# Performance work log

Measured on AMD Instinct MI355X. Metric: run time of the kernel, lower is better.

## Reference

```python
import jax, jax.numpy as jnp
import numpy as np

S = 2048       # seq_len
D = 1024       # d_model
H = 16         # heads
DK = 64        # d_k = d_v = D // H


def setup_inputs() -> dict:
    key = jax.random.key(0)
    ks = jax.random.split(key, 12)
    sc_in = 1.0 / np.sqrt(D)
    return {
        "Q": jax.random.normal(ks[0], (S, D), jnp.float32),
        "K": jax.random.normal(ks[1], (S, D), jnp.float32),
        "V": jax.random.normal(ks[2], (S, D), jnp.float32),
        # stacked per-head projection weights (torch Linear math: x @ W + b, W stored [in,out])
        "Wq": jax.random.normal(ks[3], (H, D, DK), jnp.float32) * sc_in,
        "bq": jnp.zeros((H, DK), jnp.float32),
        "Wk": jax.random.normal(ks[4], (H, D, DK), jnp.float32) * sc_in,
        "bk": jnp.zeros((H, DK), jnp.float32),
        "Wv": jax.random.normal(ks[5], (H, D, DK), jnp.float32) * sc_in,
        "bv": jnp.zeros((H, DK), jnp.float32),
        "Wo": jax.random.normal(ks[6], (H * DK, D), jnp.float32) * (1.0 / np.sqrt(H * DK)),
        "bo": jnp.zeros((D,), jnp.float32),
    }


def reference(Q, K, V, Wq, bq, Wk, bk, Wv, bv, Wo, bo):
    # per-head projections, all heads at once: [S,D] x [H,D,DK] -> [H,S,DK]
    q = jnp.einsum("sd,hdk->hsk", Q, Wq) + bq[:, None, :]
    k = jnp.einsum("sd,hdk->hsk", K, Wk) + bk[:, None, :]
    v = jnp.einsum("sd,hdk->hsk", V, Wv) + bv[:, None, :]
    # scaled dot-product attention per head: [H,S,S]
    scores = jnp.einsum("hsk,htk->hst", q, k) / jnp.sqrt(jnp.asarray(DK, q.dtype))
    attn = jax.nn.softmax(scores, axis=-1)
    heads = jnp.einsum("hst,htv->hsv", attn, v)          # [H,S,DK]
    concat = heads.transpose(1, 0, 2).reshape(S, H * DK)  # [S, H*DK]
    return concat @ Wo + bo                               # [S, D]
```

## Files before the change

kernel.cpp:

```cpp
#include <hip/hip_runtime.h>
#include <stdint.h>

#define S_LEN 2048
#define D_MODEL 1024
#define NH 16
#define DKV 64

typedef unsigned short u16;
typedef __bf16 bf16x8 __attribute__((ext_vector_type(8)));
typedef float f32x4 __attribute__((ext_vector_type(4)));

__device__ __forceinline__ u16 f2bf(float f) {
  union { float f; uint32_t u; } v; v.f = f;
  uint32_t r = v.u + 0x7FFFu + ((v.u >> 16) & 1u);
  return (u16)(r >> 16);
}
__device__ __forceinline__ uint32_t pkbf(float lo, float hi) {
  union { float f; uint32_t u; } a, b; a.f = lo; b.f = hi;
  return ((b.u + 0x8000u) & 0xFFFF0000u) | ((a.u + 0x8000u) >> 16);
}
__device__ __forceinline__ void gl16(const u16* g, u16* l) {
  __builtin_amdgcn_global_load_lds(
      (const __attribute__((address_space(1))) unsigned int*)g,
      (__attribute__((address_space(3))) unsigned int*)l, 16, 0, 0);
}

__global__ __launch_bounds__(256) void prep_k(
    const float* __restrict__ Q, const float* __restrict__ K,
    const float* __restrict__ V, const float* __restrict__ Wq,
    const float* __restrict__ Wk, const float* __restrict__ Wv,
    const float* __restrict__ Wo, u16* __restrict__ QKVb,
    u16* __restrict__ Wqt, u16* __restrict__ Wkt, u16* __restrict__ Wvt,
    u16* __restrict__ Wot) {
  __shared__ float tile[32][33];
  const int idx = blockIdx.x;
  if (idx < 6144) {
    const int z = idx >> 11, blk = idx & 2047;
    const float* src = (z == 0) ? Q : (z == 1) ? K : V;
    u16* dst = QKVb + (size_t)z * S_LEN * D_MODEL;
    size_t i = ((size_t)blk * 256 + threadIdx.x) * 4;
    const float4 v = *(const float4*)(src + i);
    union { u16 h[4]; uint2 u2; } o;
    o.h[0] = f2bf(v.x); o.h[1] = f2bf(v.y); o.h[2] = f2bf(v.z); o.h[3] = f2bf(v.w);
    *(uint2*)(dst + i) = o.u2;
    return;
  }
  const float* ip; u16* op; int R, C, r0, c0;
  if (idx < 9216) {
    int t = idx - 6144;
    int which = t >> 10, head = (t & 1023) >> 6, tl = t & 63;
    ip = ((which == 0) ? Wq : (which == 1) ? Wk : Wv) + (size_t)head * D_MODEL * DKV;
    op = ((which == 0) ? Wqt : (which == 1) ? Wkt : Wvt) + (size_t)head * D_MODEL * DKV;
    R = D_MODEL; C = DKV; c0 = (tl & 1) * 32; r0 = (tl >> 1) * 32;
  } else {
    int t = idx - 9216;
    ip = Wo; op = Wot; R = D_MODEL; C = D_MODEL;
    c0 = (t & 31) * 32; r0 = (t >> 5) * 32;
  }
  int tr = threadIdx.x >> 5, tc = threadIdx.x & 31;
#pragma unroll
  for (int i = 0; i < 4; i++)
    tile[tr + i * 8][tc] = ip[(size_t)(r0 + tr + i * 8) * C + c0 + tc];
  __syncthreads();
#pragma unroll
  for (int i = 0; i < 4; i++) {
    int c = tr + i * 8;
    op[(size_t)(c0 + c) * R + r0 + tc] = f2bf(tile[tc][c]);
  }
}

__global__ __launch_bounds__(256, 2) void proj_gemm_k(
    const u16* __restrict__ qkvb, const u16* __restrict__ Wqt,
    const u16* __restrict__ Wkt, const u16* __restrict__ Wvt,
    const float* __restrict__ bq, const float* __restrict__ bk,
    const float* __restrict__ bv,
    u16* __restrict__ qb, u16* __restrict__ kb, u16* __restrict__ vT) {
  const int bid = blockIdx.x;
  const int l = (bid & 7) * 48 + (bid >> 3);
  const int z = l >> 7, rem = l & 127;
  const int m0 = (rem >> 3) * 128, n0 = (rem & 7) * 128;
  const u16* A = qkvb + (size_t)z * S_LEN * D_MODEL;
  const u16* Bt = (z == 0) ? Wqt : (z == 1) ? Wkt : Wvt;
  const float* bias = (z == 0) ? bq : (z == 1) ? bk : bv;
  const float scale = (z == 0) ? 0.18033688f : 1.0f;

  __shared__ __align__(16) u16 smem[4 * 8192];
  const int tid = threadIdx.x;
  const int w = tid >> 6, lane = tid & 63, quad = lane >> 4, l15 = lane & 15;
  const int wm = (w >> 1) * 64, wn = (w & 1) * 64;
  const int pb = w * 256;

  f32x4 acc[4][4] = {};

  {
    u16* As = smem; u16* Bs = smem + 16384;
#pragma unroll
    for (int e = 0; e < 4; e++) {
      int p = pb + e * 64 + lane;
      int r = p >> 3, cg = (p & 7) ^ (r & 7);
      gl16(&A[(size_t)(m0 + r) * D_MODEL + cg * 8], As + (pb + e * 64) * 8);
      gl16(&Bt[(size_t)(n0 + r) * D_MODEL + cg * 8], Bs + (pb + e * 64) * 8);
    }
  }
  for (int it = 0; it < 16; it++) {
    __syncthreads();
    if (it < 15) {
      const int k0 = (it + 1) * 64;
      u16* As = smem + ((it + 1) & 1) * 8192;
      u16* Bs = smem + 16384 + ((it + 1) & 1) * 8192;
#pragma unroll
      for (int e = 0; e < 4; e++) {
        int p = pb + e * 64 + lane;
        int r = p >> 3, cg = (p & 7) ^ (r & 7);
        gl16(&A[(size_t)(m0 + r) * D_MODEL + k0 + cg * 8], As + (pb + e * 64) * 8);
        gl16(&Bt[(size_t)(n0 + r) * D_MODEL + k0 + cg * 8], Bs + (pb + e * 64) * 8);
      }
    }
    const u16* As = smem + (it & 1) * 8192;
    const u16* Bs = smem + 16384 + (it & 1) * 8192;
#pragma unroll
    for (int kc = 0; kc < 2; kc++) {
      bf16x8 af[4], bfr[4];
      const int c = kc * 4 + quad;
#pragma unroll
      for (int t = 0; t < 4; t++) {
        int ma = wm + t * 16 + l15, na = wn + t * 16 + l15;
        af[t] = *(const bf16x8*)&As[(ma * 8 + (c ^ (ma & 7))) * 8];
        bfr[t] = *(const bf16x8*)&Bs[(na * 8 + (c ^ (na & 7))) * 8];
      }
#pragma unroll
      for (int tm = 0; tm < 4; tm++)
#pragma unroll
        for (int tn = 0; tn < 4; tn++)
          acc[tm][tn] = __builtin_amdgcn_mfma_f32_16x16x32_bf16(af[tm], bfr[tn], acc[tm][tn], 0, 0, 0);
    }
  }

  if (z < 2) {
    u16* O = (z == 0) ? qb : kb;
#pragma unroll
    for (int tm = 0; tm < 4; tm++)
#pragma unroll
      for (int tn = 0; tn < 4; tn++)
#pragma unroll
        for (int r = 0; r < 4; r++) {
          int row = m0 + wm + tm * 16 + quad * 4 + r;
          int col = n0 + wn + tn * 16 + l15;
          O[(size_t)row * D_MODEL + col] = f2bf((acc[tm][tn][r] + bias[col]) * scale);
        }
  } else {
#pragma unroll
    for (int tm = 0; tm < 4; tm++)
#pragma unroll
      for (int tn = 0; tn < 4; tn++) {
        int col = n0 + wn + tn * 16 + l15;
        int row0 = m0 + wm + tm * 16 + quad * 4;
        float b = bias[col];
        union { u16 h[4]; uint2 u2; } o;
#pragma unroll
        for (int r = 0; r < 4; r++) o.h[r] = f2bf(acc[tm][tn][r] + b);
        *(uint2*)&vT[(size_t)col * S_LEN + row0] = o.u2;
      }
  }
}

__global__ __launch_bounds__(512) void attn_k(
    const u16* __restrict__ qb, const u16* __restrict__ kb,
    const u16* __restrict__ vT, u16* __restrict__ conc) {
  const int bid = blockIdx.x;
  const int l = (bid & 7) * 64 + (bid >> 3);
  const int h = l >> 5, qblk = (l & 31) * 64;
  const int tid = threadIdx.x;
  const int w = tid >> 6, lane = tid & 63, quad = lane >> 4, l15 = lane & 15;
  const int half = w >> 2, wq = w & 3;
  const int q0 = qblk + wq * 16;

  __shared__ __align__(16) u16 smem[33792];
  u16* Kh = smem + half * 6144;
  u16* Vh = smem + 12288 + half * 6144;
  u16* Pw = smem + 24576 + w * 1152;

  bf16x8 qf[2];
#pragma unroll
  for (int kc = 0; kc < 2; kc++)
    qf[kc] = *(const bf16x8*)&qb[(size_t)(q0 + l15) * D_MODEL + h * 64 + kc * 32 + quad * 8];

  const u16* kbase = kb + (size_t)h * 64;
  const u16* vbase = vT + (size_t)(h * 64) * S_LEN;

  const int p = wq * 64 + lane;
  const int kr = p >> 3, kcg = (p & 7) ^ (kr & 7);
  const int vr = p >> 2, vcg = (p & 3) ^ (vr & 3);
  const size_t kgoff = (size_t)kr * D_MODEL + kcg * 8;
  const size_t vgoff = (size_t)vr * S_LEN + vcg * 8;
  const int ldsoff = wq * 64 * 8;

  f32x4 oacc[4] = {};
  float lsum = 0.f;

  {
    const int t0 = half * 1024;
    gl16(kbase + (size_t)t0 * D_MODEL + kgoff, Kh + ldsoff);
    gl16(vbase + t0 + vgoff, Vh + ldsoff);
    const int t1 = t0 + 32;
    gl16(kbase + (size_t)t1 * D_MODEL + kgoff, Kh + 2048 + ldsoff);
    gl16(vbase + t1 + vgoff, Vh + 2048 + ldsoff);
  }

#pragma unroll
  for (int it = 0; it < 32; it++) {
    const int rd = it % 3;
    if (it < 31) asm volatile("s_waitcnt vmcnt(2)" ::: "memory");
    else         asm volatile("s_waitcnt vmcnt(0)" ::: "memory");
    __builtin_amdgcn_s_barrier();
    __builtin_amdgcn_sched_barrier(0);
    if (it < 30) {
      const int wr = (rd + 2) % 3;
      const int t0n = half * 1024 + (it + 2) * 32;
      gl16(kbase + (size_t)t0n * D_MODEL + kgoff, Kh + wr * 2048 + ldsoff);
      gl16(vbase + t0n + vgoff, Vh + wr * 2048 + ldsoff);
    }
    const u16* Kc = Kh + rd * 2048;
    const u16* Vc = Vh + rd * 2048;

    f32x4 sacc[2] = {};
    __builtin_amdgcn_s_setprio(1);
#pragma unroll
    for (int kc = 0; kc < 2; kc++)
#pragma unroll
      for (int tn = 0; tn < 2; tn++) {
        int rr = tn * 16 + l15;
        bf16x8 ka = *(const bf16x8*)&Kc[(rr * 8 + ((kc * 4 + quad) ^ (rr & 7))) * 8];
        sacc[tn] = __builtin_amdgcn_mfma_f32_16x16x32_bf16(ka, qf[kc], sacc[tn], 0, 0, 0);
      }
    __builtin_amdgcn_s_setprio(0);

#pragma unroll
    for (int tn = 0; tn < 2; tn++) {
      float p0 = __builtin_amdgcn_exp2f(sacc[tn][0]);
      float p1 = __builtin_amdgcn_exp2f(sacc[tn][1]);
      float p2 = __builtin_amdgcn_exp2f(sacc[tn][2]);
      float p3 = __builtin_amdgcn_exp2f(sacc[tn][3]);
      lsum += (p0 + p1) + (p2 + p3);
      uint2 pw2; pw2.x = pkbf(p0, p1); pw2.y = pkbf(p2, p3);
      *(uint2*)&Pw[l15 * 72 + tn * 16 + quad * 4] = pw2;
    }

    bf16x8 pa = *(const bf16x8*)&Pw[l15 * 72 + quad * 8];
    __builtin_amdgcn_s_setprio(1);
#pragma unroll
    for (int nt = 0; nt < 4; nt++) {
      int dv = nt * 16 + l15;
      bf16x8 vb = *(const bf16x8*)&Vc[(dv * 4 + (quad ^ (dv & 3))) * 8];
      oacc[nt] = __builtin_amdgcn_mfma_f32_16x16x32_bf16(pa, vb, oacc[nt], 0, 0, 0);
    }
    __builtin_amdgcn_s_setprio(0);
  }
  __syncthreads();

  lsum += __shfl_xor(lsum, 16, 64);
  lsum += __shfl_xor(lsum, 32, 64);

  float* OshF = (float*)smem;
  float* lshF = OshF + 8 * 16 * 68;
  if (lane < 16) lshF[w * 16 + lane] = lsum;
#pragma unroll
  for (int nt = 0; nt < 4; nt++)
#pragma unroll
    for (int r = 0; r < 4; r++)
      OshF[w * 1088 + (quad * 4 + r) * 68 + nt * 16 + l15] = oacc[nt][r];
  __syncthreads();

  const int q = tid >> 3;
  const int dv0 = (tid & 7) * 8;
  const int wa = q >> 4, wb = wa + 4, qr = q & 15;
  const float* pa = &OshF[wa * 1088 + qr * 68 + dv0];
  const float* pb = &OshF[wb * 1088 + qr * 68 + dv0];
  float4 a0 = *(const float4*)pa, a1 = *(const float4*)(pa + 4);
  float4 b0 = *(const float4*)pb, b1 = *(const float4*)(pb + 4);
  float li = 1.0f / (lshF[wa * 16 + qr] + lshF[wb * 16 + qr]);
  union { u16 hh[8]; uint4 u4; } o;
  o.hh[0] = f2bf((a0.x + b0.x) * li); o.hh[1] = f2bf((a0.y + b0.y) * li);
  o.hh[2] = f2bf((a0.z + b0.z) * li); o.hh[3] = f2bf((a0.w + b0.w) * li);
  o.hh[4] = f2bf((a1.x + b1.x) * li); o.hh[5] = f2bf((a1.y + b1.y) * li);
  o.hh[6] = f2bf((a1.z + b1.z) * li); o.hh[7] = f2bf((a1.w + b1.w) * li);
  *(uint4*)&conc[(size_t)(qblk + q) * D_MODEL + h * 64 + dv0] = o.u4;
}

__global__ __launch_bounds__(256, 2) void out_gemm_k(
    const u16* __restrict__ A, const u16* __restrict__ Bt,
    const float* __restrict__ bias, float* __restrict__ out) {
  const int bid = blockIdx.x;
  const int l = (bid & 7) * 64 + (bid >> 3);
  const int m0 = (l >> 4) * 64, n0 = (l & 15) * 64;
  __shared__ __align__(16) u16 smem[6 * 4096];
  const int tid = threadIdx.x;
  const int w = tid >> 6, lane = tid & 63, quad = lane >> 4, l15 = lane & 15;
  const int wm = (w >> 1) * 32, wn = (w & 1) * 32;
  const int pb = w * 128;

  f32x4 acc[2][2] = {};
  {
#pragma unroll
    for (int e = 0; e < 2; e++) {
      int p = pb + e * 64 + lane;
      int r = p >> 3, cg = (p & 7) ^ (r & 7);
      gl16(&A[(size_t)(m0 + r) * D_MODEL + cg * 8], smem + (pb + e * 64) * 8);
      gl16(&Bt[(size_t)(n0 + r) * D_MODEL + cg * 8], smem + 12288 + (pb + e * 64) * 8);
    }
#pragma unroll
    for (int e = 0; e < 2; e++) {
      int p = pb + e * 64 + lane;
      int r = p >> 3, cg = (p & 7) ^ (r & 7);
      gl16(&A[(size_t)(m0 + r) * D_MODEL + 64 + cg * 8], smem + 4096 + (pb + e * 64) * 8);
      gl16(&Bt[(size_t)(n0 + r) * D_MODEL + 64 + cg * 8], smem + 16384 + (pb + e * 64) * 8);
    }
  }
#pragma unroll
  for (int it = 0; it < 16; it++) {
    const int rd = it % 3;
    if (it < 15) asm volatile("s_waitcnt vmcnt(4)" ::: "memory");
    else         asm volatile("s_waitcnt vmcnt(0)" ::: "memory");
    __builtin_amdgcn_s_barrier();
    __builtin_amdgcn_sched_barrier(0);
    if (it < 14) {
      const int wr = (rd + 2) % 3;
      const int k0 = (it + 2) * 64;
      u16* As = smem + wr * 4096;
      u16* Bs = smem + 12288 + wr * 4096;
#pragma unroll
      for (int e = 0; e < 2; e++) {
        int p = pb + e * 64 + lane;
        int r = p >> 3, cg = (p & 7) ^ (r & 7);
        gl16(&A[(size_t)(m0 + r) * D_MODEL + k0 + cg * 8], As + (pb + e * 64) * 8);
        gl16(&Bt[(size_t)(n0 + r) * D_MODEL + k0 + cg * 8], Bs + (pb + e * 64) * 8);
      }
    }
    const u16* As = smem + rd * 4096;
    const u16* Bs = smem + 12288 + rd * 4096;
#pragma unroll
    for (int kc = 0; kc < 2; kc++) {
      const int c = kc * 4 + quad;
      bf16x8 af[2], bfr[2];
#pragma unroll
      for (int t = 0; t < 2; t++) {
        int ma = wm + t * 16 + l15, na = wn + t * 16 + l15;
        af[t] = *(const bf16x8*)&As[(ma * 8 + (c ^ (ma & 7))) * 8];
        bfr[t] = *(const bf16x8*)&Bs[(na * 8 + (c ^ (na & 7))) * 8];
      }
      __builtin_amdgcn_s_setprio(1);
#pragma unroll
      for (int tm = 0; tm < 2; tm++)
#pragma unroll
        for (int tn = 0; tn < 2; tn++)
          acc[tm][tn] = __builtin_amdgcn_mfma_f32_16x16x32_bf16(af[tm], bfr[tn], acc[tm][tn], 0, 0, 0);
      __builtin_amdgcn_s_setprio(0);
    }
  }
#pragma unroll
  for (int tm = 0; tm < 2; tm++)
#pragma unroll
    for (int tn = 0; tn < 2; tn++)
#pragma unroll
      for (int r = 0; r < 4; r++) {
        int row = m0 + wm + tm * 16 + quad * 4 + r;
        int col = n0 + wn + tn * 16 + l15;
        out[(size_t)row * D_MODEL + col] = acc[tm][tn][r] + bias[col];
      }
}

extern "C" void kernel_launch(void* const* d_in, const int* in_sizes, int n_in,
                              void* d_out, int out_size, void* d_ws, size_t ws_size,
                              hipStream_t stream) {
  const float* Q  = (const float*)d_in[0];
  const float* K  = (const float*)d_in[1];
  const float* V  = (const float*)d_in[2];
  const float* Wq = (const float*)d_in[3];
  const float* bq = (const float*)d_in[4];
  const float* Wk = (const float*)d_in[5];
  const float* bk = (const float*)d_in[6];
  const float* Wv = (const float*)d_in[7];
  const float* bv = (const float*)d_in[8];
  const float* Wo = (const float*)d_in[9];
  const float* bo = (const float*)d_in[10];
  float* out = (float*)d_out;

  u16* ws = (u16*)d_ws;
  u16* QKVb = ws;
  u16* Wqt  = QKVb + (size_t)3 * S_LEN * D_MODEL;
  u16* Wkt  = Wqt + (size_t)D_MODEL * D_MODEL;
  u16* Wvt  = Wkt + (size_t)D_MODEL * D_MODEL;
  u16* Wot  = Wvt + (size_t)D_MODEL * D_MODEL;
  u16* qbuf = Wot + (size_t)D_MODEL * D_MODEL;
  u16* kbuf = qbuf + (size_t)S_LEN * D_MODEL;
  u16* vTb  = kbuf + (size_t)S_LEN * D_MODEL;
  u16* conc = vTb + (size_t)S_LEN * D_MODEL;

  prep_k<<<dim3(10240), 256, 0, stream>>>(Q, K, V, Wq, Wk, Wv, Wo,
                                          QKVb, Wqt, Wkt, Wvt, Wot);
  proj_gemm_k<<<dim3(384), 256, 0, stream>>>(
      QKVb, Wqt, Wkt, Wvt, bq, bk, bv, qbuf, kbuf, vTb);
  attn_k<<<dim3(512), 512, 0, stream>>>(qbuf, kbuf, vTb, conc);
  out_gemm_k<<<dim3(512), 256, 0, stream>>>(conc, Wot, bo, out);
}
```

Baseline: 156.9 us.

## Use 128x64 tiles and triple-buffered prefetch in projection GEMM

New measurement: 156.3 us. Within noise of the previous version (-0.4%).

```diff
diff --git a/kernel.cpp b/kernel.cpp
--- a/kernel.cpp
+++ b/kernel.cpp
@@ -76,63 +76,90 @@
     const float* __restrict__ bv,
     u16* __restrict__ qb, u16* __restrict__ kb, u16* __restrict__ vT) {
   const int bid = blockIdx.x;
-  const int l = (bid & 7) * 48 + (bid >> 3);
-  const int z = l >> 7, rem = l & 127;
-  const int m0 = (rem >> 3) * 128, n0 = (rem & 7) * 128;
+  const int l = (bid & 7) * 96 + (bid >> 3);
+  const int z = l >> 8, rem = l & 255;
+  const int m0 = (rem >> 4) * 128, n0 = (rem & 15) * 64;
   const u16* A = qkvb + (size_t)z * S_LEN * D_MODEL;
   const u16* Bt = (z == 0) ? Wqt : (z == 1) ? Wkt : Wvt;
   const float* bias = (z == 0) ? bq : (z == 1) ? bk : bv;
   const float scale = (z == 0) ? 0.18033688f : 1.0f;
 
-  __shared__ __align__(16) u16 smem[4 * 8192];
+  __shared__ __align__(16) u16 smem[36864];
   const int tid = threadIdx.x;
   const int w = tid >> 6, lane = tid & 63, quad = lane >> 4, l15 = lane & 15;
-  const int wm = (w >> 1) * 64, wn = (w & 1) * 64;
-  const int pb = w * 256;
-
-  f32x4 acc[4][4] = {};
+  const int wm = (w >> 1) * 64, wn = (w & 1) * 32;
+  const int pbA = w * 256, pbB = w * 128;
+
+  f32x4 acc[4][2] = {};
 
   {
-    u16* As = smem; u16* Bs = smem + 16384;
-#pragma unroll
-    for (int e = 0; e < 4; e++) {
-      int p = pb + e * 64 + lane;
-      int r = p >> 3, cg = (p & 7) ^ (r & 7);
-      gl16(&A[(size_t)(m0 + r) * D_MODEL + cg * 8], As + (pb + e * 64) * 8);
-      gl16(&Bt[(size_t)(n0 + r) * D_MODEL + cg * 8], Bs + (pb + e * 64) * 8);
-    }
-  }
+#pragma unroll
+    for (int b = 0; b < 2; b++) {
+      const int k0 = b * 64;
+      u16* As = smem + b * 8192;
+      u16* Bs = smem + 24576 + b * 4096;
+#pragma unroll
+      for (int e = 0; e < 4; e++) {
+        int p = pbA + e * 64 + lane;
+        int r = p >> 3, cg = (p & 7) ^ (r & 7);
+        gl16(&A[(size_t)(m0 + r) * D_MODEL + k0 + cg * 8], As + (pbA + e * 64) * 8);
+      }
+#pragma unroll
+      for (int e = 0; e < 2; e++) {
+        int p = pbB + e * 64 + lane;
+        int r = p >> 3, cg = (p & 7) ^ (r & 7);
+        gl16(&Bt[(size_t)(n0 + r) * D_MODEL + k0 + cg * 8], Bs + (pbB + e * 64) * 8);
+      }
+    }
+  }
+#pragma unroll
   for (int it = 0; it < 16; it++) {
-    __syncthreads();
-    if (it < 15) {
-      const int k0 = (it + 1) * 64;
-      u16* As = smem + ((it + 1) & 1) * 8192;
-      u16* Bs = smem + 16384 + ((it + 1) & 1) * 8192;
+    const int rd = it % 3;
+    if (it < 15) asm volatile("s_waitcnt vmcnt(6)" ::: "memory");
+    else         asm volatile("s_waitcnt vmcnt(0)" ::: "memory");
+    __builtin_amdgcn_s_barrier();
+    __builtin_amdgcn_sched_barrier(0);
+    if (it < 14) {
+      const int wr = (rd + 2) % 3;
+      const int k0 = (it + 2) * 64;
+      u16* As = smem + wr * 8192;
+      u16* Bs = smem + 24576 + wr * 4096;
 #pragma unroll
       for (int e = 0; e < 4; e++) {
-        int p = pb + e * 64 + lane;
+        int p = pbA + e * 64 + lane;
         int r = p >> 3, cg = (p & 7) ^ (r & 7);
-        gl16(&A[(size_t)(m0 + r) * D_MODEL + k0 + cg * 8], As + (pb + e * 64) * 8);
-        gl16(&Bt[(size_t)(n0 + r) * D_MODEL + k0 + cg * 8], Bs + (pb + e * 64) * 8);
-      }
-    }
-    const u16* As = smem + (it & 1) * 8192;
-    const u16* Bs = smem + 16384 + (it & 1) * 8192;
+        gl16(&A[(size_t)(m0 + r) * D_MODEL + k0 + cg * 8], As + (pbA + e * 64) * 8);
+      }
+#pragma unroll
+      for (int e = 0; e < 2; e++) {
+        int p = pbB + e * 64 + lane;
+        int r = p >> 3, cg = (p & 7) ^ (r & 7);
+        gl16(&Bt[(size_t)(n0 + r) * D_MODEL + k0 + cg * 8], Bs + (pbB + e * 64) * 8);
+      }
+    }
+    const u16* As = smem + rd * 8192;
+    const u16* Bs = smem + 24576 + rd * 4096;
 #pragma unroll
     for (int kc = 0; kc < 2; kc++) {
-      bf16x8 af[4], bfr[4];
+      bf16x8 af[4], bfr[2];
       const int c = kc * 4 + quad;
 #pragma unroll
       for (int t = 0; t < 4; t++) {
-        int ma = wm + t * 16 + l15, na = wn + t * 16 + l15;
+        int ma = wm + t * 16 + l15;
         af[t] = *(const bf16x8*)&As[(ma * 8 + (c ^ (ma & 7))) * 8];
+      }
+#pragma unroll
+      for (int t = 0; t < 2; t++) {
+        int na = wn + t * 16 + l15;
         bfr[t] = *(const bf16x8*)&Bs[(na * 8 + (c ^ (na & 7))) * 8];
       }
+      __builtin_amdgcn_s_setprio(1);
 #pragma unroll
       for (int tm = 0; tm < 4; tm++)
 #pragma unroll
-        for (int tn = 0; tn < 4; tn++)
+        for (int tn = 0; tn < 2; tn++)
           acc[tm][tn] = __builtin_amdgcn_mfma_f32_16x16x32_bf16(af[tm], bfr[tn], acc[tm][tn], 0, 0, 0);
+      __builtin_amdgcn_s_setprio(0);
     }
   }
 
@@ -141,7 +168,7 @@
 #pragma unroll
     for (int tm = 0; tm < 4; tm++)
 #pragma unroll
-      for (int tn = 0; tn < 4; tn++)
+      for (int tn = 0; tn < 2; tn++)
 #pragma unroll
         for (int r = 0; r < 4; r++) {
           int row = m0 + wm + tm * 16 + quad * 4 + r;
@@ -152,7 +179,7 @@
 #pragma unroll
     for (int tm = 0; tm < 4; tm++)
 #pragma unroll
-      for (int tn = 0; tn < 4; tn++) {
+      for (int tn = 0; tn < 2; tn++) {
         int col = n0 + wn + tn * 16 + l15;
         int row0 = m0 + wm + tm * 16 + quad * 4;
         float b = bias[col];
@@ -398,7 +425,7 @@
 
   prep_k<<<dim3(10240), 256, 0, stream>>>(Q, K, V, Wq, Wk, Wv, Wo,
                                           QKVb, Wqt, Wkt, Wvt, Wot);
-  proj_gemm_k<<<dim3(384), 256, 0, stream>>>(
+  proj_gemm_k<<<dim3(768), 256, 0, stream>>>(
       QKVb, Wqt, Wkt, Wvt, bq, bk, bv, qbuf, kbuf, vTb);
   attn_k<<<dim3(512), 512, 0, stream>>>(qbuf, kbuf, vTb, conc);
   out_gemm_k<<<dim3(512), 256, 0, stream>>>(conc, Wot, bo, out);
```
